# Optimization experiments

Hardware: AMD Instinct MI355X
Metric: run time of the kernel (lower is better)

Reference implementation:

```python
import jax, jax.numpy as jnp
import numpy as np

N_SUBS = 64
INPUT_DIMS = 256
MIDDLE_DIMS = 128
OUTPUT_DIMS = 256
N = 131072


def setup_inputs() -> dict:
    key = jax.random.key(0)
    k1, k2 = jax.random.split(key)
    x = jax.random.normal(k1, (N, INPUT_DIMS), dtype=jnp.float32)
    sub = jax.random.randint(k2, (N,), 0, N_SUBS, dtype=jnp.int64 if jax.config.jax_enable_x64 else jnp.int32)
    # learned scalar params, initialized as in the torch module
    Gamma = jnp.ones((1,), jnp.float32) / (MIDDLE_DIMS * INPUT_DIMS)
    Lambda = jnp.ones((1,), jnp.float32) / (OUTPUT_DIMS * (INPUT_DIMS + MIDDLE_DIMS))
    return {"x": x, "sub": sub, "Gamma": Gamma, "Lambda": Lambda}


def reference(x, sub, Gamma, Lambda):
    # per-subject mean via fused segment reduction (replaces python loop)
    sums = jax.ops.segment_sum(x, sub, num_segments=N_SUBS)                      # [S, D_in]
    counts = jax.ops.segment_sum(jnp.ones((x.shape[0],), x.dtype), sub,
                                 num_segments=N_SUBS)[:, None]                    # [S, 1]
    # torch fallback for empty group: mean over row 0 of x
    means = jnp.where(counts > 0, sums / jnp.maximum(counts, 1), x[0][None, :])   # [S, D_in]
    # F.linear with rank-1 all-Gamma weight == Gamma * row-sum broadcast to middle dims
    s = jax.nn.relu(Gamma[0] * jnp.sum(means, axis=1, keepdims=True))             # [S, 1]
    stats = jnp.broadcast_to(s, (N_SUBS, MIDDLE_DIMS))                            # [S, D_mid]
    batch_stats = stats[sub]                                                      # [N, D_mid] gather
    cat = jnp.concatenate([x, batch_stats], axis=1)                               # [N, D_in+D_mid]
    o = jax.nn.relu(Lambda[0] * jnp.sum(cat, axis=1, keepdims=True))              # [N, 1]
    return jnp.broadcast_to(o, (x.shape[0], OUTPUT_DIMS))                         # [N, D_out]
```

## Files before the change

kernel.cpp:

```cpp
#include <hip/hip_runtime.h>

#define N_ROWS   131072
#define D_IN     256
#define D_MID    128
#define N_SUBS   64

#define K1_BLOCKS      2048
#define K1_THREADS     256
#define K1_WAVES       (K1_BLOCKS * K1_THREADS / 64)
#define K1_ROWS_PER_W  (N_ROWS / K1_WAVES)

#define K2_BLOCKS      256
#define K2_THREADS     1024
#define K2_WAVES       (K2_BLOCKS * K2_THREADS / 64)
#define K2_ROWS_PER_W  (N_ROWS / K2_WAVES)


__global__ __launch_bounds__(256) void k1_rowsum_bins(const float* __restrict__ x,
                                                      const int* __restrict__ sub,
                                                      float* __restrict__ rowsum,
                                                      float* __restrict__ partials) {
    __shared__ float ls[2 * N_SUBS];
    if (threadIdx.x < 2 * N_SUBS) ls[threadIdx.x] = 0.0f;
    __syncthreads();

    int wave = (blockIdx.x * K1_THREADS + threadIdx.x) >> 6;
    int lane = threadIdx.x & 63;

    #pragma unroll 4
    for (int r = 0; r < K1_ROWS_PER_W; ++r) {
        int row = wave + r * K1_WAVES;
        float4 v = ((const float4*)(x + (size_t)row * D_IN))[lane];
        float s = (v.x + v.y) + (v.z + v.w);
        #pragma unroll
        for (int m = 32; m >= 1; m >>= 1) s += __shfl_xor(s, m, 64);
        if (lane == 0) {
            rowsum[row] = s;
            int g = sub[row];
            atomicAdd(&ls[g], s);
            atomicAdd(&ls[N_SUBS + g], 1.0f);
        }
    }
    __syncthreads();
    if (threadIdx.x < 2 * N_SUBS)
        partials[(size_t)blockIdx.x * (2 * N_SUBS) + threadIdx.x] = ls[threadIdx.x];
}

__global__ __launch_bounds__(1024) void k2_out(const float* __restrict__ rowsum,
                                               const int* __restrict__ sub,
                                               const float* __restrict__ partials,
                                               const float* __restrict__ Gamma,
                                               const float* __restrict__ Lambda,
                                               float* __restrict__ out) {
    __shared__ float red[8][2 * N_SUBS];
    __shared__ float tg[N_SUBS];
    int tid = threadIdx.x;

    {
        int slot  = tid & 127;
        int chunk = tid >> 7;
        float acc = 0.0f;
        int b0 = chunk * (K1_BLOCKS / 8);
        for (int b = b0; b < b0 + (K1_BLOCKS / 8); ++b)
            acc += partials[(size_t)b * (2 * N_SUBS) + slot];
        red[chunk][slot] = acc;
    }
    __syncthreads();
    if (tid < 2 * N_SUBS) {
        float t0 = 0.0f;
        #pragma unroll
        for (int c = 0; c < 8; ++c) t0 += red[c][tid];
        red[0][tid] = t0;
    }
    __syncthreads();
    if (tid < N_SUBS) {
        float sum = red[0][tid];
        float cnt = red[0][N_SUBS + tid];
        float meansum = (cnt > 0.0f) ? (sum / cnt) : rowsum[0];
        float s = Gamma[0] * meansum;
        s = s > 0.0f ? s : 0.0f;
        tg[tid] = Lambda[0] * (float)D_MID * s;
    }
    __syncthreads();

    float lam  = Lambda[0];
    int gw   = (blockIdx.x * K2_THREADS + tid) >> 6;
    int lane = tid & 63;

    #pragma unroll 4
    for (int r = 0; r < K2_ROWS_PER_W; ++r) {
        int row = gw + r * K2_WAVES;
        float o = lam * rowsum[row] + tg[sub[row]];
        o = o > 0.0f ? o : 0.0f;
        ((float4*)(out + (size_t)row * D_IN))[lane] = make_float4(o, o, o, o);
    }
}

extern "C" void kernel_launch(void* const* d_in, const int* in_sizes, int n_in,
                              void* d_out, int out_size, void* d_ws, size_t ws_size,
                              hipStream_t stream) {
    const float* x      = (const float*)d_in[0];
    const int*   sub    = (const int*)d_in[1];
    const float* Gamma  = (const float*)d_in[2];
    const float* Lambda = (const float*)d_in[3];
    float* out = (float*)d_out;

    float* rowsum   = (float*)d_ws;
    float* partials = rowsum + N_ROWS;

    k1_rowsum_bins<<<K1_BLOCKS, K1_THREADS, 0, stream>>>(x, sub, rowsum, partials);
    k2_out<<<K2_BLOCKS, K2_THREADS, 0, stream>>>(rowsum, sub, partials, Gamma, Lambda, out);
}
```

Baseline: 269.9 us.

## Fuse rowsum and output kernels into one cooperative kernel with grid sync

Merges the two kernels into a single cooperative launch of 1024 blocks that computes row sums and per-subject bins, grid-syncs, reduces partials in parallel across 128 blocks (transposed partials layout), grid-syncs again, then writes the broadcast output. The aim is to remove the second launch and the serial partials reduction that every block of the old second kernel repeated. The cost is two grid-wide barriers and the cooperative-launch residency limit.

```diff
diff --git a/kernel.cpp b/kernel.cpp
--- a/kernel.cpp
+++ b/kernel.cpp
@@ -1,35 +1,40 @@
 #include <hip/hip_runtime.h>
+#include <hip/hip_cooperative_groups.h>
+
+namespace cg = cooperative_groups;
 
 #define N_ROWS   131072
 #define D_IN     256
 #define D_MID    128
 #define N_SUBS   64
 
-#define K1_BLOCKS      2048
-#define K1_THREADS     256
-#define K1_WAVES       (K1_BLOCKS * K1_THREADS / 64)
-#define K1_ROWS_PER_W  (N_ROWS / K1_WAVES)
-
-#define K2_BLOCKS      256
-#define K2_THREADS     1024
-#define K2_WAVES       (K2_BLOCKS * K2_THREADS / 64)
-#define K2_ROWS_PER_W  (N_ROWS / K2_WAVES)
+#define NBLK     1024
+#define NTHR     256
+#define NWAVE    (NBLK * NTHR / 64)
+#define RPW      (N_ROWS / NWAVE)
 
 
-__global__ __launch_bounds__(256) void k1_rowsum_bins(const float* __restrict__ x,
-                                                      const int* __restrict__ sub,
-                                                      float* __restrict__ rowsum,
-                                                      float* __restrict__ partials) {
+__global__ __launch_bounds__(NTHR, 4) void fused(const float* __restrict__ x,
+                                                 const int* __restrict__ sub,
+                                                 const float* __restrict__ Gamma,
+                                                 const float* __restrict__ Lambda,
+                                                 float* __restrict__ out,
+                                                 float* __restrict__ rowsum,
+                                                 float* __restrict__ partials,
+                                                 float* __restrict__ gfin) {
+    cg::grid_group grid = cg::this_grid();
     __shared__ float ls[2 * N_SUBS];
-    if (threadIdx.x < 2 * N_SUBS) ls[threadIdx.x] = 0.0f;
+    __shared__ float tg[N_SUBS];
+    int tid  = threadIdx.x;
+    int lane = tid & 63;
+    int gwave = (blockIdx.x * NTHR + tid) >> 6;
+
+    if (tid < 2 * N_SUBS) ls[tid] = 0.0f;
     __syncthreads();
 
-    int wave = (blockIdx.x * K1_THREADS + threadIdx.x) >> 6;
-    int lane = threadIdx.x & 63;
-
     #pragma unroll 4
-    for (int r = 0; r < K1_ROWS_PER_W; ++r) {
-        int row = wave + r * K1_WAVES;
+    for (int r = 0; r < RPW; ++r) {
+        int row = gwave + r * NWAVE;
         float4 v = ((const float4*)(x + (size_t)row * D_IN))[lane];
         float s = (v.x + v.y) + (v.z + v.w);
         #pragma unroll
@@ -42,40 +47,25 @@
         }
     }
     __syncthreads();
-    if (threadIdx.x < 2 * N_SUBS)
-        partials[(size_t)blockIdx.x * (2 * N_SUBS) + threadIdx.x] = ls[threadIdx.x];
-}
+    if (tid < 2 * N_SUBS) partials[(size_t)tid * NBLK + blockIdx.x] = ls[tid];
+    __threadfence();
+    grid.sync();
 
-__global__ __launch_bounds__(1024) void k2_out(const float* __restrict__ rowsum,
-                                               const int* __restrict__ sub,
-                                               const float* __restrict__ partials,
-                                               const float* __restrict__ Gamma,
-                                               const float* __restrict__ Lambda,
-                                               float* __restrict__ out) {
-    __shared__ float red[8][2 * N_SUBS];
-    __shared__ float tg[N_SUBS];
-    int tid = threadIdx.x;
+    if (blockIdx.x < 2 * N_SUBS) {
+        const float* src = partials + (size_t)blockIdx.x * NBLK;
+        float a = src[tid] + src[tid + 256] + src[tid + 512] + src[tid + 768];
+        #pragma unroll
+        for (int m = 32; m >= 1; m >>= 1) a += __shfl_xor(a, m, 64);
+        if (lane == 0) ls[tid >> 6] = a;
+        __syncthreads();
+        if (tid == 0) gfin[blockIdx.x] = ls[0] + ls[1] + ls[2] + ls[3];
+    }
+    __threadfence();
+    grid.sync();
 
-    {
-        int slot  = tid & 127;
-        int chunk = tid >> 7;
-        float acc = 0.0f;
-        int b0 = chunk * (K1_BLOCKS / 8);
-        for (int b = b0; b < b0 + (K1_BLOCKS / 8); ++b)
-            acc += partials[(size_t)b * (2 * N_SUBS) + slot];
-        red[chunk][slot] = acc;
-    }
-    __syncthreads();
-    if (tid < 2 * N_SUBS) {
-        float t0 = 0.0f;
-        #pragma unroll
-        for (int c = 0; c < 8; ++c) t0 += red[c][tid];
-        red[0][tid] = t0;
-    }
-    __syncthreads();
     if (tid < N_SUBS) {
-        float sum = red[0][tid];
-        float cnt = red[0][N_SUBS + tid];
+        float sum = gfin[tid];
+        float cnt = gfin[N_SUBS + tid];
         float meansum = (cnt > 0.0f) ? (sum / cnt) : rowsum[0];
         float s = Gamma[0] * meansum;
         s = s > 0.0f ? s : 0.0f;
@@ -83,13 +73,10 @@
     }
     __syncthreads();
 
-    float lam  = Lambda[0];
-    int gw   = (blockIdx.x * K2_THREADS + tid) >> 6;
-    int lane = tid & 63;
-
+    float lam = Lambda[0];
     #pragma unroll 4
-    for (int r = 0; r < K2_ROWS_PER_W; ++r) {
-        int row = gw + r * K2_WAVES;
+    for (int r = 0; r < RPW; ++r) {
+        int row = gwave + r * NWAVE;
         float o = lam * rowsum[row] + tg[sub[row]];
         o = o > 0.0f ? o : 0.0f;
         ((float4*)(out + (size_t)row * D_IN))[lane] = make_float4(o, o, o, o);
@@ -107,7 +94,9 @@
 
     float* rowsum   = (float*)d_ws;
     float* partials = rowsum + N_ROWS;
+    float* gfin     = partials + 2 * N_SUBS * NBLK;
 
-    k1_rowsum_bins<<<K1_BLOCKS, K1_THREADS, 0, stream>>>(x, sub, rowsum, partials);
-    k2_out<<<K2_BLOCKS, K2_THREADS, 0, stream>>>(rowsum, sub, partials, Gamma, Lambda, out);
+    void* args[] = {(void*)&x, (void*)&sub, (void*)&Gamma, (void*)&Lambda,
+                    (void*)&out, (void*)&rowsum, (void*)&partials, (void*)&gfin};
+    hipLaunchCooperativeKernel((void*)fused, dim3(NBLK), dim3(NTHR), args, 0, stream);
 }
```

Measured after the change: 640.5 us. 2.37x slower.
